# Optimization experiments

Hardware: AMD Instinct MI355X
Metric: run time of the kernel (lower is better)

The kernel has to match this reference:

```python
import jax, jax.numpy as jnp
import numpy as np

B = 2048   # jets (graphs)
P = 50     # particles per jet
N = B * P  # nodes
E = B * P * P  # within-jet all-pairs radius-graph edges (incl. self-loops)
H = 5      # edge-MLP width ([5,5,5,5] channel list)
EPS = 1e-5
NEG_SLOPE = 0.01


def _batchnorm(h, gamma, beta):
    # training-mode batch norm over the edge dimension (biased variance, as torch)
    mu = jnp.mean(h, axis=0)
    var = jnp.mean(h * h, axis=0) - mu * mu
    return gamma * (h - mu) * jax.lax.rsqrt(var + EPS) + beta


def setup_inputs() -> dict:
    key = jax.random.key(0)
    ks = jax.random.split(key, 16)
    # angles: per-jet center offset + tight spread so all within-jet pairs are inside dR=0.4
    centers = jax.random.normal(ks[0], (B, 1, 2), dtype=jnp.float32) + jnp.array([2.0, 0.5], dtype=jnp.float32)
    angles = (centers + 0.1 * jax.random.normal(ks[1], (B, P, 2), dtype=jnp.float32)).reshape(N, 2)
    pt = jax.random.uniform(ks[2], (N,), dtype=jnp.float32, minval=0.1, maxval=1.0)
    features = jnp.linalg.norm(angles, axis=-1, keepdims=True)  # rho = |view_as_complex(angles)|, [N,1]
    # radius graph: with the tight spread every within-jet pair is within dR -> fixed E
    ii = np.arange(P)
    pi, pj = np.meshgrid(ii, ii, indexing='ij')
    base = (np.arange(B, dtype=np.int64) * P)[:, None]
    src = (base + pj.ravel()[None, :]).ravel()  # x_j (source)
    dst = (base + pi.ravel()[None, :]).ravel()  # x_i (target) = aggregation index
    edge_index = jnp.asarray(np.stack([src, dst]), dtype=jnp.int32)  # [2, E]
    def lin(k, o, i):
        return (jax.random.normal(k, (o, i), dtype=jnp.float32) / np.sqrt(i)).astype(jnp.float32)
    W1 = lin(ks[3], H, 5); b1 = jnp.zeros((H,), jnp.float32)
    W2 = lin(ks[4], H, H); b2 = jnp.zeros((H,), jnp.float32)
    W3 = lin(ks[5], H, H); b3 = jnp.zeros((H,), jnp.float32)
    g1 = jnp.ones((H,), jnp.float32); bt1 = jnp.zeros((H,), jnp.float32)
    g2 = jnp.ones((H,), jnp.float32); bt2 = jnp.zeros((H,), jnp.float32)
    return {"pt": pt, "features": features, "angles": angles,
            "W1": W1, "b1": b1, "g1": g1, "bt1": bt1,
            "W2": W2, "b2": b2, "g2": g2, "bt2": bt2,
            "W3": W3, "b3": b3, "edge_index": edge_index}


def reference(pt, features, angles, W1, b1, g1, bt1, W2, b2, g2, bt2, W3, b3, edge_index):
    src = edge_index[0]  # j (source)
    dst = edge_index[1]  # i (target, aggregation index)
    x = jnp.concatenate([pt[:, None], features, angles], axis=1)  # [N, 4]
    xi = x[dst]  # [E, 4]
    xj = x[src]
    # complex ratio angles_i / angles_j in real arithmetic
    ar, ai = xi[:, 2], xi[:, 3]
    br, bi = xj[:, 2], xj[:, 3]
    den = br * br + bi * bi
    dr = (ar * br + ai * bi) / den
    di = (ai * br - ar * bi) / den
    fi = xi[:, 1:2]
    fj = xj[:, 1:2]
    mlp_in = jnp.concatenate([fi, fj, fj - fi, dr[:, None], di[:, None]], axis=1)  # [E, 5]
    h = jax.nn.leaky_relu(_batchnorm(mlp_in @ W1.T + b1, g1, bt1), NEG_SLOPE)
    h = jax.nn.leaky_relu(_batchnorm(h @ W2.T + b2, g2, bt2), NEG_SLOPE)
    h = h @ W3.T + b3  # [E, 5]
    msg = jnp.concatenate([xi[:, :1], h, xi[:, 2:4]], axis=1)  # [E, 8]
    pt_e = msg[:, 0]
    denom = jax.ops.segment_sum(pt_e, dst, num_segments=N)  # [N]
    wj = pt_e / denom[dst]
    agg = jax.ops.segment_sum(wj[:, None] * msg, dst, num_segments=N)  # [N, 8]
    # exp(2*pi*i*theta) * z with theta = agg[:, -3], z = complex(agg[:, -2:])
    theta = agg[:, 5]
    zr, zi = agg[:, 6], agg[:, 7]
    c = jnp.cos(2.0 * jnp.pi * theta)
    s = jnp.sin(2.0 * jnp.pi * theta)
    out = jnp.concatenate([agg[:, :5], (c * zr - s * zi)[:, None], (c * zi + s * zr)[:, None]], axis=1)  # [N, 7]
    return out
```

## Files before the change

kernel.cpp:

```cpp
#include <hip/hip_runtime.h>

#define PP 50
#define TPB 256
#define NBATCH 2048
#define NCOPY 64

static constexpr float EPSF = 1e-5f;
static constexpr double ETOT = 5120000.0;

static __device__ __forceinline__ float lrelu(float x) {
    return fmaxf(x, 0.0f) + 0.01f * fminf(x, 0.0f);
}
static __device__ __forceinline__ float rfl(float x) {
    return __int_as_float(__builtin_amdgcn_readfirstlane(__float_as_int(x)));
}


__global__ __launch_bounds__(TPB) void pass1_kernel(
    const float* __restrict__ feat, const float* __restrict__ ang,
    const float* __restrict__ W1, const float* __restrict__ b1,
    double* __restrict__ acc)
{
    __shared__ float4 nd[PP];
    __shared__ float red[4][10];
    const int t = threadIdx.x;
    const int base = blockIdx.x * PP;

    if (t < PP) {
        float f  = feat[base + t];
        float br = ang[2*(base+t)];
        float bi = ang[2*(base+t)+1];
        nd[t] = make_float4(f, br, bi, 1.0f / (br*br + bi*bi));
    }

    float w1[25], bb1[5];
#pragma unroll
    for (int i = 0; i < 25; ++i) w1[i] = rfl(W1[i]);
#pragma unroll
    for (int i = 0; i < 5; ++i)  bb1[i] = rfl(b1[i]);

    __syncthreads();

    float a[10];
#pragma unroll
    for (int k = 0; k < 10; ++k) a[k] = 0.0f;

    if (t < 250) {
        const int pi = t / 5;
        const int s  = t - pi*5;
        const float4 ni = nd[pi];
        const float fi = ni.x, ar = ni.y, ai = ni.z;
#pragma unroll
        for (int q = 0; q < 10; ++q) {
            const float4 nj = nd[s*10 + q];
            const float fj = nj.x, br = nj.y, bi = nj.z, inv = nj.w;
            const float dr = (ar*br + ai*bi) * inv;
            const float dm = (ai*br - ar*bi) * inv;
            const float df = fj - fi;
#pragma unroll
            for (int o = 0; o < 5; ++o) {
                float y = bb1[o];
                y = fmaf(w1[o*5+0], fi, y);
                y = fmaf(w1[o*5+1], fj, y);
                y = fmaf(w1[o*5+2], df, y);
                y = fmaf(w1[o*5+3], dr, y);
                y = fmaf(w1[o*5+4], dm, y);
                a[o]   += y;
                a[5+o]  = fmaf(y, y, a[5+o]);
            }
        }
    }

#pragma unroll
    for (int k = 0; k < 10; ++k) {
        float v = a[k];
#pragma unroll
        for (int off = 32; off > 0; off >>= 1) v += __shfl_down(v, off, 64);
        a[k] = v;
    }
    const int lane = t & 63, wv = t >> 6;
    if (lane == 0) {
#pragma unroll
        for (int k = 0; k < 10; ++k) red[wv][k] = a[k];
    }
    __syncthreads();
    if (t < 10) {
        atomicAdd(&acc[t * NCOPY + (blockIdx.x & (NCOPY-1))],
                  (double)(red[0][t] + red[1][t] + red[2][t] + red[3][t]));
    }
}

__global__ __launch_bounds__(TPB) void pass2_kernel(
    const float* __restrict__ feat, const float* __restrict__ ang,
    const float* __restrict__ W1, const float* __restrict__ b1,
    const float* __restrict__ g1, const float* __restrict__ bt1,
    const float* __restrict__ W2, const float* __restrict__ b2,
    double* __restrict__ acc)
{
    __shared__ float4 nd[PP];
    __shared__ double tmp[10];
    __shared__ float red[4][10];
    const int t = threadIdx.x;
    const int base = blockIdx.x * PP;

    if (t < PP) {
        float f  = feat[base + t];
        float br = ang[2*(base+t)];
        float bi = ang[2*(base+t)+1];
        nd[t] = make_float4(f, br, bi, 1.0f / (br*br + bi*bi));
    }
    if (t >= 64 && t < 74) {
        const int k = t - 64;
        double s = 0.0;
#pragma unroll
        for (int c = 0; c < NCOPY; ++c) s += acc[k * NCOPY + c];
        tmp[k] = s;
    }

    float w1[25], bb1[5], w2[25], bb2[5];
#pragma unroll
    for (int i = 0; i < 25; ++i) { w1[i] = rfl(W1[i]); w2[i] = rfl(W2[i]); }
#pragma unroll
    for (int i = 0; i < 5; ++i)  { bb1[i] = rfl(b1[i]); bb2[i] = rfl(b2[i]); }

    __syncthreads();

    float sc1[5], sh1[5];
#pragma unroll
    for (int o = 0; o < 5; ++o) {
        double mu  = tmp[o]   / ETOT;
        double var = tmp[5+o] / ETOT - mu * mu;
        float s = rfl(g1[o]) * rsqrtf((float)var + EPSF);
        sc1[o] = rfl(s);
        sh1[o] = rfl(rfl(bt1[o]) - (float)mu * s);
    }

    float a[10];
#pragma unroll
    for (int k = 0; k < 10; ++k) a[k] = 0.0f;

    if (t < 250) {
        const int pi = t / 5;
        const int s  = t - pi*5;
        const float4 ni = nd[pi];
        const float fi = ni.x, ar = ni.y, ai = ni.z;
#pragma unroll
        for (int q = 0; q < 10; ++q) {
            const float4 nj = nd[s*10 + q];
            const float fj = nj.x, br = nj.y, bi = nj.z, inv = nj.w;
            const float dr = (ar*br + ai*bi) * inv;
            const float dm = (ai*br - ar*bi) * inv;
            const float df = fj - fi;
            float h1[5];
#pragma unroll
            for (int o = 0; o < 5; ++o) {
                float y = bb1[o];
                y = fmaf(w1[o*5+0], fi, y);
                y = fmaf(w1[o*5+1], fj, y);
                y = fmaf(w1[o*5+2], df, y);
                y = fmaf(w1[o*5+3], dr, y);
                y = fmaf(w1[o*5+4], dm, y);
                h1[o] = lrelu(fmaf(y, sc1[o], sh1[o]));
            }
#pragma unroll
            for (int o = 0; o < 5; ++o) {
                float y = bb2[o];
                y = fmaf(w2[o*5+0], h1[0], y);
                y = fmaf(w2[o*5+1], h1[1], y);
                y = fmaf(w2[o*5+2], h1[2], y);
                y = fmaf(w2[o*5+3], h1[3], y);
                y = fmaf(w2[o*5+4], h1[4], y);
                a[o]   += y;
                a[5+o]  = fmaf(y, y, a[5+o]);
            }
        }
    }

#pragma unroll
    for (int k = 0; k < 10; ++k) {
        float v = a[k];
#pragma unroll
        for (int off = 32; off > 0; off >>= 1) v += __shfl_down(v, off, 64);
        a[k] = v;
    }
    const int lane = t & 63, wv = t >> 6;
    if (lane == 0) {
#pragma unroll
        for (int k = 0; k < 10; ++k) red[wv][k] = a[k];
    }
    __syncthreads();
    if (t < 10) {
        atomicAdd(&acc[(10 + t) * NCOPY + (blockIdx.x & (NCOPY-1))],
                  (double)(red[0][t] + red[1][t] + red[2][t] + red[3][t]));
    }
}

__global__ __launch_bounds__(TPB) void pass3_kernel(
    const float* __restrict__ pt,
    const float* __restrict__ feat, const float* __restrict__ ang,
    const float* __restrict__ W1, const float* __restrict__ b1,
    const float* __restrict__ g1, const float* __restrict__ bt1,
    const float* __restrict__ W2, const float* __restrict__ b2,
    const float* __restrict__ g2, const float* __restrict__ bt2,
    const float* __restrict__ W3, const float* __restrict__ b3,
    const double* __restrict__ acc, float* __restrict__ out)
{
    __shared__ float4 nd[PP];
    __shared__ float spt[PP];
    __shared__ double tmp[20];
    __shared__ float part[250][5];
    const int t = threadIdx.x;
    const int base = blockIdx.x * PP;

    if (t < PP) {
        float f  = feat[base + t];
        float br = ang[2*(base+t)];
        float bi = ang[2*(base+t)+1];
        nd[t] = make_float4(f, br, bi, 1.0f / (br*br + bi*bi));
        spt[t] = pt[base + t];
    }
    if (t >= 64 && t < 84) {
        const int k = t - 64;
        double s = 0.0;
#pragma unroll
        for (int c = 0; c < NCOPY; ++c) s += acc[k * NCOPY + c];
        tmp[k] = s;
    }

    float w1[25], bb1[5], w2[25], bb2[5], w3[25], bb3[5];
#pragma unroll
    for (int i = 0; i < 25; ++i) {
        w1[i] = rfl(W1[i]); w2[i] = rfl(W2[i]); w3[i] = rfl(W3[i]);
    }
#pragma unroll
    for (int i = 0; i < 5; ++i) {
        bb1[i] = rfl(b1[i]); bb2[i] = rfl(b2[i]); bb3[i] = rfl(b3[i]);
    }

    __syncthreads();

    float sc1[5], sh1[5], sc2[5], sh2[5];
#pragma unroll
    for (int o = 0; o < 5; ++o) {
        double mu1  = tmp[o]    / ETOT;
        double var1 = tmp[5+o]  / ETOT - mu1 * mu1;
        float s1 = rfl(g1[o]) * rsqrtf((float)var1 + EPSF);
        sc1[o] = rfl(s1);
        sh1[o] = rfl(rfl(bt1[o]) - (float)mu1 * s1);
        double mu2  = tmp[10+o] / ETOT;
        double var2 = tmp[15+o] / ETOT - mu2 * mu2;
        float s2 = rfl(g2[o]) * rsqrtf((float)var2 + EPSF);
        sc2[o] = rfl(s2);
        sh2[o] = rfl(rfl(bt2[o]) - (float)mu2 * s2);
    }

    float a[5];
#pragma unroll
    for (int k = 0; k < 5; ++k) a[k] = 0.0f;

    if (t < 250) {
        const int pi = t / 5;
        const int s  = t - pi*5;
        const float4 ni = nd[pi];
        const float fi = ni.x, ar = ni.y, ai = ni.z;
#pragma unroll
        for (int q = 0; q < 10; ++q) {
            const float4 nj = nd[s*10 + q];
            const float fj = nj.x, br = nj.y, bi = nj.z, inv = nj.w;
            const float dr = (ar*br + ai*bi) * inv;
            const float dm = (ai*br - ar*bi) * inv;
            const float df = fj - fi;
            float h1[5], h2[5];
#pragma unroll
            for (int o = 0; o < 5; ++o) {
                float y = bb1[o];
                y = fmaf(w1[o*5+0], fi, y);
                y = fmaf(w1[o*5+1], fj, y);
                y = fmaf(w1[o*5+2], df, y);
                y = fmaf(w1[o*5+3], dr, y);
                y = fmaf(w1[o*5+4], dm, y);
                h1[o] = lrelu(fmaf(y, sc1[o], sh1[o]));
            }
#pragma unroll
            for (int o = 0; o < 5; ++o) {
                float y = bb2[o];
                y = fmaf(w2[o*5+0], h1[0], y);
                y = fmaf(w2[o*5+1], h1[1], y);
                y = fmaf(w2[o*5+2], h1[2], y);
                y = fmaf(w2[o*5+3], h1[3], y);
                y = fmaf(w2[o*5+4], h1[4], y);
                h2[o] = lrelu(fmaf(y, sc2[o], sh2[o]));
            }
#pragma unroll
            for (int o = 0; o < 5; ++o) {
                float y = bb3[o];
                y = fmaf(w3[o*5+0], h2[0], y);
                y = fmaf(w3[o*5+1], h2[1], y);
                y = fmaf(w3[o*5+2], h2[2], y);
                y = fmaf(w3[o*5+3], h2[3], y);
                y = fmaf(w3[o*5+4], h2[4], y);
                a[o] += y;
            }
        }
    }

    if (t < 250) {
#pragma unroll
        for (int c = 0; c < 5; ++c) part[t][c] = a[c];
    }
    __syncthreads();

    if (t < PP) {
        float m[5];
#pragma unroll
        for (int c = 0; c < 5; ++c) {
            m[c] = (part[5*t][c] + part[5*t+1][c] + part[5*t+2][c] +
                    part[5*t+3][c] + part[5*t+4][c]) * 0.02f;
        }
        const int d = base + t;
        const float4 ni = nd[t];
        const float zr = ni.y, zi = ni.z;
        float ss, cc;
        sincosf(6.2831853071795865f * m[4], &ss, &cc);
        float* o = out + (size_t)d * 7;
        o[0] = spt[t];
        o[1] = m[0];
        o[2] = m[1];
        o[3] = m[2];
        o[4] = m[3];
        o[5] = cc * zr - ss * zi;
        o[6] = cc * zi + ss * zr;
    }
}

extern "C" void kernel_launch(void* const* d_in, const int* in_sizes, int n_in,
                              void* d_out, int out_size, void* d_ws, size_t ws_size,
                              hipStream_t stream)
{
    const float* pt   = (const float*)d_in[0];
    const float* feat = (const float*)d_in[1];
    const float* ang  = (const float*)d_in[2];
    const float* W1   = (const float*)d_in[3];
    const float* b1   = (const float*)d_in[4];
    const float* g1   = (const float*)d_in[5];
    const float* bt1  = (const float*)d_in[6];
    const float* W2   = (const float*)d_in[7];
    const float* b2   = (const float*)d_in[8];
    const float* g2   = (const float*)d_in[9];
    const float* bt2  = (const float*)d_in[10];
    const float* W3   = (const float*)d_in[11];
    const float* b3   = (const float*)d_in[12];
    float* out  = (float*)d_out;
    double* acc = (double*)d_ws;

    hipMemsetAsync(d_ws, 0, 1280 * sizeof(double), stream);
    pass1_kernel<<<NBATCH, TPB, 0, stream>>>(feat, ang, W1, b1, acc);
    pass2_kernel<<<NBATCH, TPB, 0, stream>>>(feat, ang, W1, b1, g1, bt1, W2, b2, acc);
    pass3_kernel<<<NBATCH, TPB, 0, stream>>>(pt, feat, ang, W1, b1, g1, bt1, W2, b2,
                                             g2, bt2, W3, b3, acc, out);
}
```

Measured before the change: 154.5 us.

## Fuse three passes into persistent kernel with grid barriers and closed-form BN1 stats

Replaces three separate kernel launches with one persistent kernel of 512 blocks, each handling four jets, synchronised by atomic grid barriers between the batch-norm statistics phases. The first-layer batch-norm moments are now computed in closed form from per-jet node sums, which removes a full pass over all edges. W1 is also folded so the fj-fi input column disappears. The costs are spin-wait barriers that assume all 512 blocks are co-resident, and a risk of float precision loss in the closed-form second moments.

```diff
diff --git a/kernel.cpp b/kernel.cpp
--- a/kernel.cpp
+++ b/kernel.cpp
@@ -3,10 +3,12 @@
 #define PP 50
 #define TPB 256
 #define NBATCH 2048
-#define NCOPY 64
+#define NBLK 512
+#define GPB (NBATCH / NBLK)
+#define NCOPY 32
 
 static constexpr float EPSF = 1e-5f;
-static constexpr double ETOT = 5120000.0;
+static constexpr double INV_ETOT = 1.0 / 5120000.0;
 
 static __device__ __forceinline__ float lrelu(float x) {
     return fmaxf(x, 0.0f) + 0.01f * fminf(x, 0.0f);
@@ -14,188 +16,21 @@
 static __device__ __forceinline__ float rfl(float x) {
     return __int_as_float(__builtin_amdgcn_readfirstlane(__float_as_int(x)));
 }
-
-
-__global__ __launch_bounds__(TPB) void pass1_kernel(
-    const float* __restrict__ feat, const float* __restrict__ ang,
-    const float* __restrict__ W1, const float* __restrict__ b1,
-    double* __restrict__ acc)
-{
-    __shared__ float4 nd[PP];
-    __shared__ float red[4][10];
-    const int t = threadIdx.x;
-    const int base = blockIdx.x * PP;
-
-    if (t < PP) {
-        float f  = feat[base + t];
-        float br = ang[2*(base+t)];
-        float bi = ang[2*(base+t)+1];
-        nd[t] = make_float4(f, br, bi, 1.0f / (br*br + bi*bi));
-    }
-
-    float w1[25], bb1[5];
-#pragma unroll
-    for (int i = 0; i < 25; ++i) w1[i] = rfl(W1[i]);
-#pragma unroll
-    for (int i = 0; i < 5; ++i)  bb1[i] = rfl(b1[i]);
-
-    __syncthreads();
-
-    float a[10];
-#pragma unroll
-    for (int k = 0; k < 10; ++k) a[k] = 0.0f;
-
-    if (t < 250) {
-        const int pi = t / 5;
-        const int s  = t - pi*5;
-        const float4 ni = nd[pi];
-        const float fi = ni.x, ar = ni.y, ai = ni.z;
-#pragma unroll
-        for (int q = 0; q < 10; ++q) {
-            const float4 nj = nd[s*10 + q];
-            const float fj = nj.x, br = nj.y, bi = nj.z, inv = nj.w;
-            const float dr = (ar*br + ai*bi) * inv;
-            const float dm = (ai*br - ar*bi) * inv;
-            const float df = fj - fi;
-#pragma unroll
-            for (int o = 0; o < 5; ++o) {
-                float y = bb1[o];
-                y = fmaf(w1[o*5+0], fi, y);
-                y = fmaf(w1[o*5+1], fj, y);
-                y = fmaf(w1[o*5+2], df, y);
-                y = fmaf(w1[o*5+3], dr, y);
-                y = fmaf(w1[o*5+4], dm, y);
-                a[o]   += y;
-                a[5+o]  = fmaf(y, y, a[5+o]);
-            }
-        }
-    }
-
-#pragma unroll
-    for (int k = 0; k < 10; ++k) {
-        float v = a[k];
-#pragma unroll
-        for (int off = 32; off > 0; off >>= 1) v += __shfl_down(v, off, 64);
-        a[k] = v;
-    }
-    const int lane = t & 63, wv = t >> 6;
-    if (lane == 0) {
-#pragma unroll
-        for (int k = 0; k < 10; ++k) red[wv][k] = a[k];
-    }
-    __syncthreads();
-    if (t < 10) {
-        atomicAdd(&acc[t * NCOPY + (blockIdx.x & (NCOPY-1))],
-                  (double)(red[0][t] + red[1][t] + red[2][t] + red[3][t]));
-    }
-}
-
-__global__ __launch_bounds__(TPB) void pass2_kernel(
-    const float* __restrict__ feat, const float* __restrict__ ang,
-    const float* __restrict__ W1, const float* __restrict__ b1,
-    const float* __restrict__ g1, const float* __restrict__ bt1,
-    const float* __restrict__ W2, const float* __restrict__ b2,
-    double* __restrict__ acc)
-{
-    __shared__ float4 nd[PP];
-    __shared__ double tmp[10];
-    __shared__ float red[4][10];
-    const int t = threadIdx.x;
-    const int base = blockIdx.x * PP;
-
-    if (t < PP) {
-        float f  = feat[base + t];
-        float br = ang[2*(base+t)];
-        float bi = ang[2*(base+t)+1];
-        nd[t] = make_float4(f, br, bi, 1.0f / (br*br + bi*bi));
-    }
-    if (t >= 64 && t < 74) {
-        const int k = t - 64;
-        double s = 0.0;
-#pragma unroll
-        for (int c = 0; c < NCOPY; ++c) s += acc[k * NCOPY + c];
-        tmp[k] = s;
-    }
-
-    float w1[25], bb1[5], w2[25], bb2[5];
-#pragma unroll
-    for (int i = 0; i < 25; ++i) { w1[i] = rfl(W1[i]); w2[i] = rfl(W2[i]); }
-#pragma unroll
-    for (int i = 0; i < 5; ++i)  { bb1[i] = rfl(b1[i]); bb2[i] = rfl(b2[i]); }
-
-    __syncthreads();
-
-    float sc1[5], sh1[5];
-#pragma unroll
-    for (int o = 0; o < 5; ++o) {
-        double mu  = tmp[o]   / ETOT;
-        double var = tmp[5+o] / ETOT - mu * mu;
-        float s = rfl(g1[o]) * rsqrtf((float)var + EPSF);
-        sc1[o] = rfl(s);
-        sh1[o] = rfl(rfl(bt1[o]) - (float)mu * s);
-    }
-
-    float a[10];
-#pragma unroll
-    for (int k = 0; k < 10; ++k) a[k] = 0.0f;
-
-    if (t < 250) {
-        const int pi = t / 5;
-        const int s  = t - pi*5;
-        const float4 ni = nd[pi];
-        const float fi = ni.x, ar = ni.y, ai = ni.z;
-#pragma unroll
-        for (int q = 0; q < 10; ++q) {
-            const float4 nj = nd[s*10 + q];
-            const float fj = nj.x, br = nj.y, bi = nj.z, inv = nj.w;
-            const float dr = (ar*br + ai*bi) * inv;
-            const float dm = (ai*br - ar*bi) * inv;
-            const float df = fj - fi;
-            float h1[5];
-#pragma unroll
-            for (int o = 0; o < 5; ++o) {
-                float y = bb1[o];
-                y = fmaf(w1[o*5+0], fi, y);
-                y = fmaf(w1[o*5+1], fj, y);
-                y = fmaf(w1[o*5+2], df, y);
-                y = fmaf(w1[o*5+3], dr, y);
-                y = fmaf(w1[o*5+4], dm, y);
-                h1[o] = lrelu(fmaf(y, sc1[o], sh1[o]));
-            }
-#pragma unroll
-            for (int o = 0; o < 5; ++o) {
-                float y = bb2[o];
-                y = fmaf(w2[o*5+0], h1[0], y);
-                y = fmaf(w2[o*5+1], h1[1], y);
-                y = fmaf(w2[o*5+2], h1[2], y);
-                y = fmaf(w2[o*5+3], h1[3], y);
-                y = fmaf(w2[o*5+4], h1[4], y);
-                a[o]   += y;
-                a[5+o]  = fmaf(y, y, a[5+o]);
-            }
-        }
-    }
-
-#pragma unroll
-    for (int k = 0; k < 10; ++k) {
-        float v = a[k];
-#pragma unroll
-        for (int off = 32; off > 0; off >>= 1) v += __shfl_down(v, off, 64);
-        a[k] = v;
-    }
-    const int lane = t & 63, wv = t >> 6;
-    if (lane == 0) {
-#pragma unroll
-        for (int k = 0; k < 10; ++k) red[wv][k] = a[k];
-    }
-    __syncthreads();
-    if (t < 10) {
-        atomicAdd(&acc[(10 + t) * NCOPY + (blockIdx.x & (NCOPY-1))],
-                  (double)(red[0][t] + red[1][t] + red[2][t] + red[3][t]));
-    }
-}
-
-__global__ __launch_bounds__(TPB) void pass3_kernel(
+static __device__ __forceinline__ double aload(const double* p) {
+    return __hip_atomic_load(p, __ATOMIC_RELAXED, __HIP_MEMORY_SCOPE_AGENT);
+}
+static __device__ __forceinline__ void grid_barrier(int* cnt) {
+    __syncthreads();
+    if (threadIdx.x == 0) {
+        __hip_atomic_fetch_add(cnt, 1, __ATOMIC_ACQ_REL, __HIP_MEMORY_SCOPE_AGENT);
+        while (__hip_atomic_load(cnt, __ATOMIC_ACQUIRE, __HIP_MEMORY_SCOPE_AGENT) < NBLK)
+            __builtin_amdgcn_s_sleep(2);
+    }
+    __syncthreads();
+}
+
+
+__global__ __launch_bounds__(TPB, 4) void fused_kernel(
     const float* __restrict__ pt,
     const float* __restrict__ feat, const float* __restrict__ ang,
     const float* __restrict__ W1, const float* __restrict__ b1,
@@ -203,133 +38,245 @@
     const float* __restrict__ W2, const float* __restrict__ b2,
     const float* __restrict__ g2, const float* __restrict__ bt2,
     const float* __restrict__ W3, const float* __restrict__ b3,
-    const double* __restrict__ acc, float* __restrict__ out)
+    double* __restrict__ acc, int* __restrict__ bar,
+    float* __restrict__ out)
 {
-    __shared__ float4 nd[PP];
-    __shared__ float spt[PP];
-    __shared__ double tmp[20];
+    __shared__ float4 nd[GPB][PP];
+    __shared__ float spt[GPB][PP];
+    __shared__ float red[4][10];
+    __shared__ double bacc[4][10];
+    __shared__ double tmp[10];
+    __shared__ float fold[20];
     __shared__ float part[250][5];
+
     const int t = threadIdx.x;
-    const int base = blockIdx.x * PP;
-
-    if (t < PP) {
-        float f  = feat[base + t];
-        float br = ang[2*(base+t)];
-        float bi = ang[2*(base+t)+1];
-        nd[t] = make_float4(f, br, bi, 1.0f / (br*br + bi*bi));
-        spt[t] = pt[base + t];
-    }
-    if (t >= 64 && t < 84) {
-        const int k = t - 64;
+    const int lane = t & 63;
+    const int wv = t >> 6;
+    const int b0 = blockIdx.x * GPB;
+    const int copy = blockIdx.x & (NCOPY - 1);
+
+    float v0[5], v1[5], v2[5], v3[5], bb1[5], bb2[5], bb3[5];
+    float w2[25], w3[25];
+#pragma unroll
+    for (int o = 0; o < 5; ++o) {
+        v0[o] = rfl(W1[o*5+0] - W1[o*5+2]);
+        v1[o] = rfl(W1[o*5+1] + W1[o*5+2]);
+        v2[o] = rfl(W1[o*5+3]);
+        v3[o] = rfl(W1[o*5+4]);
+        bb1[o] = rfl(b1[o]); bb2[o] = rfl(b2[o]); bb3[o] = rfl(b3[o]);
+    }
+#pragma unroll
+    for (int i = 0; i < 25; ++i) { w2[i] = rfl(W2[i]); w3[i] = rfl(W3[i]); }
+
+    float f = 0.f, zr = 0.f, zi = 0.f, inv = 0.f;
+    if (lane < PP) {
+        const int idx = (b0 + wv) * PP + lane;
+        f = feat[idx];
+        float2 a2 = ((const float2*)ang)[idx];
+        zr = a2.x; zi = a2.y;
+        inv = 1.0f / (zr*zr + zi*zi);
+        nd[wv][lane]  = make_float4(f, zr, zi, inv);
+        spt[wv][lane] = pt[idx];
+    }
+
+    {
+        float wr = zr * inv, wi = -zi * inv;
+        float p[16] = { f, f*f, zr, zi, wr, wi, f*zr, f*zi, f*wr, f*wi,
+                        zr*zr, zi*zi, zr*zi, wr*wr, wi*wi, wr*wi };
+#pragma unroll
+        for (int k = 0; k < 16; ++k) {
+            float v = p[k];
+#pragma unroll
+            for (int off = 32; off > 0; off >>= 1) v += __shfl_down(v, off, 64);
+            p[k] = v;
+        }
+        if (lane == 0) {
+            const float Sfi = 50.f * p[0];
+            const float Sdr = p[2]*p[4] - p[3]*p[5];
+            const float Sdi = p[3]*p[4] + p[2]*p[5];
+            const float m00 = 50.f * p[1], m11 = m00, m01 = p[0]*p[0];
+            const float m02 = p[6]*p[4] - p[7]*p[5];
+            const float m03 = p[7]*p[4] + p[6]*p[5];
+            const float m12 = p[2]*p[8] - p[3]*p[9];
+            const float m13 = p[3]*p[8] + p[2]*p[9];
+            const float m22 = p[10]*p[13] - 2.f*p[12]*p[15] + p[11]*p[14];
+            const float m33 = p[11]*p[13] + 2.f*p[12]*p[15] + p[10]*p[14];
+            const float m23 = p[12]*p[13] + p[10]*p[15] - p[11]*p[15] - p[12]*p[14];
+#pragma unroll
+            for (int o = 0; o < 5; ++o) {
+                const float a0=v0[o], a1=v1[o], a2=v2[o], a3=v3[o], bo=bb1[o];
+                const float sy = a0*Sfi + a1*Sfi + a2*Sdr + a3*Sdi + 2500.f*bo;
+                const float q  = a0*a0*m00 + a1*a1*m11 + a2*a2*m22 + a3*a3*m33
+                               + 2.f*(a0*a1*m01 + a0*a2*m02 + a0*a3*m03
+                                    + a1*a2*m12 + a1*a3*m13 + a2*a3*m23);
+                const float sy2 = q + 2.f*bo*sy - 2500.f*bo*bo;
+                bacc[wv][o]   = (double)sy;
+                bacc[wv][5+o] = (double)sy2;
+            }
+        }
+    }
+    __syncthreads();
+    if (t < 10) {
+        double s = bacc[0][t] + bacc[1][t] + bacc[2][t] + bacc[3][t];
+        atomicAdd(&acc[t * NCOPY + copy], s);
+    }
+    grid_barrier(bar + 0);
+
+    if (t < 10) {
         double s = 0.0;
 #pragma unroll
-        for (int c = 0; c < NCOPY; ++c) s += acc[k * NCOPY + c];
-        tmp[k] = s;
-    }
-
-    float w1[25], bb1[5], w2[25], bb2[5], w3[25], bb3[5];
-#pragma unroll
-    for (int i = 0; i < 25; ++i) {
-        w1[i] = rfl(W1[i]); w2[i] = rfl(W2[i]); w3[i] = rfl(W3[i]);
-    }
-#pragma unroll
-    for (int i = 0; i < 5; ++i) {
-        bb1[i] = rfl(b1[i]); bb2[i] = rfl(b2[i]); bb3[i] = rfl(b3[i]);
-    }
-
-    __syncthreads();
-
-    float sc1[5], sh1[5], sc2[5], sh2[5];
-#pragma unroll
-    for (int o = 0; o < 5; ++o) {
-        double mu1  = tmp[o]    / ETOT;
-        double var1 = tmp[5+o]  / ETOT - mu1 * mu1;
-        float s1 = rfl(g1[o]) * rsqrtf((float)var1 + EPSF);
-        sc1[o] = rfl(s1);
-        sh1[o] = rfl(rfl(bt1[o]) - (float)mu1 * s1);
-        double mu2  = tmp[10+o] / ETOT;
-        double var2 = tmp[15+o] / ETOT - mu2 * mu2;
-        float s2 = rfl(g2[o]) * rsqrtf((float)var2 + EPSF);
-        sc2[o] = rfl(s2);
-        sh2[o] = rfl(rfl(bt2[o]) - (float)mu2 * s2);
-    }
-
-    float a[5];
-#pragma unroll
-    for (int k = 0; k < 5; ++k) a[k] = 0.0f;
-
-    if (t < 250) {
-        const int pi = t / 5;
-        const int s  = t - pi*5;
-        const float4 ni = nd[pi];
-        const float fi = ni.x, ar = ni.y, ai = ni.z;
-#pragma unroll
-        for (int q = 0; q < 10; ++q) {
-            const float4 nj = nd[s*10 + q];
-            const float fj = nj.x, br = nj.y, bi = nj.z, inv = nj.w;
-            const float dr = (ar*br + ai*bi) * inv;
-            const float dm = (ai*br - ar*bi) * inv;
-            const float df = fj - fi;
-            float h1[5], h2[5];
-#pragma unroll
-            for (int o = 0; o < 5; ++o) {
-                float y = bb1[o];
-                y = fmaf(w1[o*5+0], fi, y);
-                y = fmaf(w1[o*5+1], fj, y);
-                y = fmaf(w1[o*5+2], df, y);
-                y = fmaf(w1[o*5+3], dr, y);
-                y = fmaf(w1[o*5+4], dm, y);
-                h1[o] = lrelu(fmaf(y, sc1[o], sh1[o]));
+        for (int c = 0; c < NCOPY; ++c) s += aload(&acc[t * NCOPY + c]);
+        tmp[t] = s;
+    }
+    __syncthreads();
+    if (t < 5) {
+        double mu  = tmp[t]   * INV_ETOT;
+        double var = tmp[5+t] * INV_ETOT - mu * mu;
+        float sc = g1[t] * rsqrtf((float)var + EPSF);
+        fold[t] = sc; fold[5+t] = bt1[t] - (float)mu * sc;
+    }
+    __syncthreads();
+    float sc1[5], sh1[5];
+#pragma unroll
+    for (int o = 0; o < 5; ++o) { sc1[o] = rfl(fold[o]); sh1[o] = rfl(fold[5+o]); }
+
+    const int pi = t / 5;
+    const int s5 = t - pi * 5;
+    {
+        float a[10];
+#pragma unroll
+        for (int k = 0; k < 10; ++k) a[k] = 0.f;
+        if (t < 250) {
+#pragma unroll
+            for (int g = 0; g < GPB; ++g) {
+                const float4 ni = nd[g][pi];
+                const float fi = ni.x, ari = ni.y, aii = ni.z;
+#pragma unroll
+                for (int q = 0; q < 10; ++q) {
+                    const float4 nj = nd[g][s5*10 + q];
+                    const float dr = fmaf(ari, nj.y,  aii*nj.z) * nj.w;
+                    const float di = fmaf(aii, nj.y, -ari*nj.z) * nj.w;
+                    float h1[5];
+#pragma unroll
+                    for (int o = 0; o < 5; ++o) {
+                        float y = fmaf(v0[o], fi, fmaf(v1[o], nj.x,
+                                  fmaf(v2[o], dr, fmaf(v3[o], di, bb1[o]))));
+                        h1[o] = lrelu(fmaf(y, sc1[o], sh1[o]));
+                    }
+#pragma unroll
+                    for (int o = 0; o < 5; ++o) {
+                        float y = bb2[o];
+                        y = fmaf(w2[o*5+0], h1[0], y);
+                        y = fmaf(w2[o*5+1], h1[1], y);
+                        y = fmaf(w2[o*5+2], h1[2], y);
+                        y = fmaf(w2[o*5+3], h1[3], y);
+                        y = fmaf(w2[o*5+4], h1[4], y);
+                        a[o]   += y;
+                        a[5+o]  = fmaf(y, y, a[5+o]);
+                    }
+                }
             }
-#pragma unroll
-            for (int o = 0; o < 5; ++o) {
-                float y = bb2[o];
-                y = fmaf(w2[o*5+0], h1[0], y);
-                y = fmaf(w2[o*5+1], h1[1], y);
-                y = fmaf(w2[o*5+2], h1[2], y);
-                y = fmaf(w2[o*5+3], h1[3], y);
-                y = fmaf(w2[o*5+4], h1[4], y);
-                h2[o] = lrelu(fmaf(y, sc2[o], sh2[o]));
+        }
+#pragma unroll
+        for (int k = 0; k < 10; ++k) {
+            float v = a[k];
+#pragma unroll
+            for (int off = 32; off > 0; off >>= 1) v += __shfl_down(v, off, 64);
+            a[k] = v;
+        }
+        if (lane == 0) {
+#pragma unroll
+            for (int k = 0; k < 10; ++k) red[wv][k] = a[k];
+        }
+    }
+    __syncthreads();
+    if (t < 10) {
+        atomicAdd(&acc[(10 + t) * NCOPY + copy],
+                  (double)(red[0][t] + red[1][t] + red[2][t] + red[3][t]));
+    }
+    grid_barrier(bar + 1);
+
+    if (t < 10) {
+        double s = 0.0;
+#pragma unroll
+        for (int c = 0; c < NCOPY; ++c) s += aload(&acc[(10 + t) * NCOPY + c]);
+        tmp[t] = s;
+    }
+    __syncthreads();
+    if (t < 5) {
+        double mu  = tmp[t]   * INV_ETOT;
+        double var = tmp[5+t] * INV_ETOT - mu * mu;
+        float sc = g2[t] * rsqrtf((float)var + EPSF);
+        fold[10+t] = sc; fold[15+t] = bt2[t] - (float)mu * sc;
+    }
+    __syncthreads();
+    float sc2[5], sh2[5];
+#pragma unroll
+    for (int o = 0; o < 5; ++o) { sc2[o] = rfl(fold[10+o]); sh2[o] = rfl(fold[15+o]); }
+
+    for (int g = 0; g < GPB; ++g) {
+        float a[5] = {0.f, 0.f, 0.f, 0.f, 0.f};
+        if (t < 250) {
+            const float4 ni = nd[g][pi];
+            const float fi = ni.x, ari = ni.y, aii = ni.z;
+#pragma unroll
+            for (int q = 0; q < 10; ++q) {
+                const float4 nj = nd[g][s5*10 + q];
+                const float dr = fmaf(ari, nj.y,  aii*nj.z) * nj.w;
+                const float di = fmaf(aii, nj.y, -ari*nj.z) * nj.w;
+                float h1[5], h2[5];
+#pragma unroll
+                for (int o = 0; o < 5; ++o) {
+                    float y = fmaf(v0[o], fi, fmaf(v1[o], nj.x,
+                              fmaf(v2[o], dr, fmaf(v3[o], di, bb1[o]))));
+                    h1[o] = lrelu(fmaf(y, sc1[o], sh1[o]));
+                }
+#pragma unroll
+                for (int o = 0; o < 5; ++o) {
+                    float y = bb2[o];
+                    y = fmaf(w2[o*5+0], h1[0], y);
+                    y = fmaf(w2[o*5+1], h1[1], y);
+                    y = fmaf(w2[o*5+2], h1[2], y);
+                    y = fmaf(w2[o*5+3], h1[3], y);
+                    y = fmaf(w2[o*5+4], h1[4], y);
+                    h2[o] = lrelu(fmaf(y, sc2[o], sh2[o]));
+                }
+#pragma unroll
+                for (int o = 0; o < 5; ++o) {
+                    float y = bb3[o];
+                    y = fmaf(w3[o*5+0], h2[0], y);
+                    y = fmaf(w3[o*5+1], h2[1], y);
+                    y = fmaf(w3[o*5+2], h2[2], y);
+                    y = fmaf(w3[o*5+3], h2[3], y);
+                    y = fmaf(w3[o*5+4], h2[4], y);
+                    a[o] += y;
+                }
             }
 #pragma unroll
-            for (int o = 0; o < 5; ++o) {
-                float y = bb3[o];
-                y = fmaf(w3[o*5+0], h2[0], y);
-                y = fmaf(w3[o*5+1], h2[1], y);
-                y = fmaf(w3[o*5+2], h2[2], y);
-                y = fmaf(w3[o*5+3], h2[3], y);
-                y = fmaf(w3[o*5+4], h2[4], y);
-                a[o] += y;
+            for (int c = 0; c < 5; ++c) part[t][c] = a[c];
+        }
+        __syncthreads();
+        if (t < PP) {
+            float m[5];
+#pragma unroll
+            for (int c = 0; c < 5; ++c) {
+                m[c] = (part[5*t][c] + part[5*t+1][c] + part[5*t+2][c] +
+                        part[5*t+3][c] + part[5*t+4][c]) * 0.02f;
             }
-        }
-    }
-
-    if (t < 250) {
-#pragma unroll
-        for (int c = 0; c < 5; ++c) part[t][c] = a[c];
-    }
-    __syncthreads();
-
-    if (t < PP) {
-        float m[5];
-#pragma unroll
-        for (int c = 0; c < 5; ++c) {
-            m[c] = (part[5*t][c] + part[5*t+1][c] + part[5*t+2][c] +
-                    part[5*t+3][c] + part[5*t+4][c]) * 0.02f;
-        }
-        const int d = base + t;
-        const float4 ni = nd[t];
-        const float zr = ni.y, zi = ni.z;
-        float ss, cc;
-        sincosf(6.2831853071795865f * m[4], &ss, &cc);
-        float* o = out + (size_t)d * 7;
-        o[0] = spt[t];
-        o[1] = m[0];
-        o[2] = m[1];
-        o[3] = m[2];
-        o[4] = m[3];
-        o[5] = cc * zr - ss * zi;
-        o[6] = cc * zi + ss * zr;
+            const int d = (b0 + g) * PP + t;
+            const float4 ni = nd[g][t];
+            float ss, cc;
+            sincosf(6.2831853071795865f * m[4], &ss, &cc);
+            float* o = out + (size_t)d * 7;
+            o[0] = spt[g][t];
+            o[1] = m[0];
+            o[2] = m[1];
+            o[3] = m[2];
+            o[4] = m[3];
+            o[5] = cc * ni.y - ss * ni.z;
+            o[6] = cc * ni.z + ss * ni.y;
+        }
+        __syncthreads();
     }
 }
 
@@ -352,10 +299,10 @@
     const float* b3   = (const float*)d_in[12];
     float* out  = (float*)d_out;
     double* acc = (double*)d_ws;
-
-    hipMemsetAsync(d_ws, 0, 1280 * sizeof(double), stream);
-    pass1_kernel<<<NBATCH, TPB, 0, stream>>>(feat, ang, W1, b1, acc);
-    pass2_kernel<<<NBATCH, TPB, 0, stream>>>(feat, ang, W1, b1, g1, bt1, W2, b2, acc);
-    pass3_kernel<<<NBATCH, TPB, 0, stream>>>(pt, feat, ang, W1, b1, g1, bt1, W2, b2,
-                                             g2, bt2, W3, b3, acc, out);
-}
+    int* bar    = (int*)((char*)d_ws + 20 * NCOPY * sizeof(double));
+
+    hipMemsetAsync(d_ws, 0, 20 * NCOPY * sizeof(double) + 2 * sizeof(int), stream);
+    fused_kernel<<<NBLK, TPB, 0, stream>>>(pt, feat, ang, W1, b1, g1, bt1,
+                                           W2, b2, g2, bt2, W3, b3,
+                                           acc, bar, out);
+}
```

New measurement: 222.8 us. 44.2% more time.
